# Kernel optimization log

Hardware: AMD Instinct MI355X
Metric: run time of the kernel (lower is better)

## Reference

```python
import jax, jax.numpy as jnp
import numpy as np

N_NODES = 100000
N_EDGES = 1000000
D = 64


def setup_inputs() -> dict:
    key = jax.random.key(0)
    k1, k2, k3, k4, k5, k6 = jax.random.split(key, 6)
    graph_embedding = jax.random.normal(k1, (N_NODES, D), dtype=jnp.float32)
    e_feat = jax.random.randint(k2, (N_EDGES,), 0, 8, dtype=jnp.int32)
    src_idx = jax.random.randint(k3, (N_EDGES,), 0, N_NODES, dtype=jnp.int32)
    dst_idx = jax.random.randint(k4, (N_EDGES,), 0, N_NODES, dtype=jnp.int32)
    # learned parameters (xavier-uniform-like scale)
    weight = jax.random.uniform(k5, (1, D), dtype=jnp.float32, minval=-1.0, maxval=1.0) * np.sqrt(6.0 / (1 + D))
    semantic_weight = jax.random.uniform(k6, (1, 5), dtype=jnp.float32, minval=-1.0, maxval=1.0) * np.sqrt(6.0 / (1 + 5))
    return {
        "graph_embedding": graph_embedding,
        "e_feat": e_feat,
        "src_idx": src_idx,
        "dst_idx": dst_idx,
        "weight": weight,
        "semantic_weight": semantic_weight,
    }


def reference(graph_embedding, e_feat, src_idx, dst_idx, weight, semantic_weight):
    n_nodes = graph_embedding.shape[0]
    # NOTE: original forward multiplies all five ft variants by the SAME self.weight
    emb = graph_embedding * weight                      # [N, D]
    src_ft = emb[src_idx]                               # [E, D] gather
    e = e_feat.astype(jnp.float32)[:, None]             # [E, 1] (e_feat.reshape(-1,1).float())
    sw = semantic_weight[0]                             # [5]
    msg = src_ft * sw[0]
    for i, ev in enumerate((0.0, 2.0, 4.0, 6.0)):
        mask = (e == ev)                                # [E, 1], broadcast over D
        msg = msg + jnp.where(mask, src_ft, jnp.zeros_like(src_ft)) * sw[i + 1]
    # scatter-sum messages into destination nodes
    out = jax.ops.segment_sum(msg, dst_idx, num_segments=n_nodes)  # [N, D]
    return out
```

## Files before the change

### kernel.cpp

```cpp
#include <hip/hip_runtime.h>


#define DIM 64
#define LOGB 7
#define NPB 128
#define NBUK_MAX 1024
#define CAP 2048
#define CHUNK 4096
#define OVF_CAP 8192

__global__ __launch_bounds__(512) void k_bin(
    const int* __restrict__ e_feat, const int* __restrict__ src_idx,
    const int* __restrict__ dst_idx,
    int* __restrict__ cursor, int* __restrict__ ovf_cnt, int4* __restrict__ ovf,
    unsigned int* __restrict__ recs, int E, int nbuk)
{
    __shared__ int hist[NBUK_MAX];
    __shared__ int start[NBUK_MAX];
    __shared__ int adjs[NBUK_MAX];
    __shared__ int partial[512];
    __shared__ unsigned int stage_rec[CHUNK];
    __shared__ unsigned short stage_b[CHUNK];

    const int t = threadIdx.x;
    const int base = blockIdx.x * CHUNK;
    int n = E - base; if (n > CHUNK) n = CHUNK;

    hist[t] = 0; hist[t + 512] = 0;
    __syncthreads();

    unsigned int rec[8]; int bk[8]; int lr[8];
    #pragma unroll
    for (int k = 0; k < 8; ++k) {
        int i = t + k * 512;
        if (i < n) {
            int j = base + i;
            int d = dst_idx[j];
            int s = src_idx[j];
            int f = e_feat[j];
            bk[k]  = d >> LOGB;
            rec[k] = (unsigned)s | ((unsigned)(d & (NPB - 1)) << 17)
                                 | ((unsigned)f << 24);
            lr[k]  = atomicAdd(&hist[bk[k]], 1);
        } else bk[k] = -1;
    }
    __syncthreads();

    int a  = hist[2 * t];
    int b2 = hist[2 * t + 1];
    partial[t] = a + b2;
    __syncthreads();
    for (int off = 1; off < 512; off <<= 1) {
        int v = (t >= off) ? partial[t - off] : 0;
        __syncthreads();
        partial[t] += v;
        __syncthreads();
    }
    int pbase = partial[t] - (a + b2);
    start[2 * t]     = pbase;
    start[2 * t + 1] = pbase + a;
    __syncthreads();

    #pragma unroll
    for (int k = 0; k < 8; ++k) {
        if (bk[k] >= 0) {
            int pos = start[bk[k]] + lr[k];
            stage_rec[pos] = rec[k];
            stage_b[pos]   = (unsigned short)bk[k];
        }
    }
    for (int b = t; b < nbuk; b += 512) {
        int c = hist[b];
        if (c > 0) {
            int g0 = atomicAdd(&cursor[b], c);
            adjs[b] = g0 - start[b];
        }
    }
    __syncthreads();

    for (int i = t; i < n; i += 512) {
        int b  = stage_b[i];
        int dp = adjs[b] + i;
        unsigned int r = stage_rec[i];
        if (dp < CAP) {
            recs[(size_t)b * CAP + dp] = r;
        } else {
            int oi = atomicAdd(ovf_cnt, 1);
            if (oi < OVF_CAP) {
                int s  = r & 0x1FFFF;
                int dl = (r >> 17) & (NPB - 1);
                int f  = (r >> 24) & 7;
                ovf[oi] = make_int4((b << LOGB) | dl, s, f, 0);
            }
        }
    }
}

__global__ __launch_bounds__(256) void k_regroup(
    const int* __restrict__ cursor, const unsigned int* __restrict__ recs,
    const float* __restrict__ sw,
    int2* __restrict__ recs2, int2* __restrict__ meta, int N)
{
    __shared__ int hist2[NPB];
    __shared__ int sc[NPB];
    __shared__ int nstart[NPB];
    __shared__ int2 rbuf[CAP];

    const int t = threadIdx.x;
    const int b = blockIdx.x;
    int cnt = cursor[b]; if (cnt > CAP) cnt = CAP;

    for (int i = t; i < NPB; i += 256) hist2[i] = 0;
    __syncthreads();

    float s0 = sw[0], s1 = sw[1], s2 = sw[2], s3 = sw[3], s4 = sw[4];

    unsigned int r[8]; int nl[8]; int lr[8];
    #pragma unroll
    for (int k = 0; k < 8; ++k) {
        int i = t + k * 256;
        if (i < cnt) {
            r[k]  = recs[(size_t)b * CAP + i];
            nl[k] = (r[k] >> 17) & (NPB - 1);
            lr[k] = atomicAdd(&hist2[nl[k]], 1);
        } else nl[k] = -1;
    }
    __syncthreads();

    if (t < NPB) sc[t] = hist2[t];
    __syncthreads();
    for (int off = 1; off < NPB; off <<= 1) {
        int v = (t < NPB && t >= off) ? sc[t - off] : 0;
        __syncthreads();
        if (t < NPB) sc[t] += v;
        __syncthreads();
    }
    if (t < NPB) nstart[t] = sc[t] - hist2[t];
    __syncthreads();

    #pragma unroll
    for (int k = 0; k < 8; ++k) {
        if (nl[k] >= 0) {
            int f = (r[k] >> 24) & 7;
            float c = s0;
            c += (f == 0) ? s1 : 0.0f;
            c += (f == 2) ? s2 : 0.0f;
            c += (f == 4) ? s3 : 0.0f;
            c += (f == 6) ? s4 : 0.0f;
            rbuf[nstart[nl[k]] + lr[k]] = make_int2((int)(r[k] & 0x1FFFF),
                                                    __float_as_int(c));
        }
    }
    __syncthreads();

    for (int i = t; i < cnt; i += 256)
        recs2[(size_t)b * CAP + i] = rbuf[i];

    const int node0 = b << LOGB;
    if (t < NPB) {
        int node = node0 + t;
        if (node < N)
            meta[node] = make_int2(b * CAP + nstart[t], hist2[t]);
    }
}

__global__ __launch_bounds__(256) void k_gather(
    const float* __restrict__ emb, const float* __restrict__ weight,
    const int2* __restrict__ meta, const int2* __restrict__ recs2,
    float* __restrict__ out, int N)
{
    int wave = threadIdx.x >> 6;
    int lane = threadIdx.x & 63;
    int node = blockIdx.x * 4 + wave;
    if (node >= N) return;

    int2 m = meta[node];
    int s = m.x, cnt = m.y;

    float a0=0.f,a1=0.f,a2=0.f,a3=0.f,a4=0.f,a5=0.f,a6=0.f,a7=0.f;

    for (int base = 0; base < cnt; base += 64) {
        int nch = cnt - base; if (nch > 64) nch = 64;
        int2 r = make_int2(0, 0);
        if (lane < nch) r = recs2[s + base + lane];
        int j = 0;
        for (; j + 7 < nch; j += 8) {
            int   s0 = __shfl(r.x, j    ), s1 = __shfl(r.x, j + 1);
            int   s2 = __shfl(r.x, j + 2), s3 = __shfl(r.x, j + 3);
            int   s4 = __shfl(r.x, j + 4), s5 = __shfl(r.x, j + 5);
            int   s6 = __shfl(r.x, j + 6), s7 = __shfl(r.x, j + 7);
            float c0 = __int_as_float(__shfl(r.y, j    ));
            float c1 = __int_as_float(__shfl(r.y, j + 1));
            float c2 = __int_as_float(__shfl(r.y, j + 2));
            float c3 = __int_as_float(__shfl(r.y, j + 3));
            float c4 = __int_as_float(__shfl(r.y, j + 4));
            float c5 = __int_as_float(__shfl(r.y, j + 5));
            float c6 = __int_as_float(__shfl(r.y, j + 6));
            float c7 = __int_as_float(__shfl(r.y, j + 7));
            a0 = fmaf(c0, emb[(size_t)s0 * DIM + lane], a0);
            a1 = fmaf(c1, emb[(size_t)s1 * DIM + lane], a1);
            a2 = fmaf(c2, emb[(size_t)s2 * DIM + lane], a2);
            a3 = fmaf(c3, emb[(size_t)s3 * DIM + lane], a3);
            a4 = fmaf(c4, emb[(size_t)s4 * DIM + lane], a4);
            a5 = fmaf(c5, emb[(size_t)s5 * DIM + lane], a5);
            a6 = fmaf(c6, emb[(size_t)s6 * DIM + lane], a6);
            a7 = fmaf(c7, emb[(size_t)s7 * DIM + lane], a7);
        }
        for (; j < nch; ++j) {
            int   sj = __shfl(r.x, j);
            float cj = __int_as_float(__shfl(r.y, j));
            a0 = fmaf(cj, emb[(size_t)sj * DIM + lane], a0);
        }
    }
    float acc = ((a0 + a1) + (a2 + a3)) + ((a4 + a5) + (a6 + a7));
    out[(size_t)node * DIM + lane] = acc * weight[lane];
}

__global__ __launch_bounds__(64) void k_overflow(
    const int* __restrict__ ovf_cnt, const int4* __restrict__ ovf,
    const float* __restrict__ emb, const float* __restrict__ weight,
    const float* __restrict__ sw, float* __restrict__ out)
{
    int m = *ovf_cnt; if (m > OVF_CAP) m = OVF_CAP;
    int lane = threadIdx.x;
    float s0 = sw[0], s1 = sw[1], s2 = sw[2], s3 = sw[3], s4 = sw[4];
    for (int i = blockIdx.x; i < m; i += gridDim.x) {
        int4 rec = ovf[i];
        int f = rec.z;
        float c = s0;
        c += (f == 0) ? s1 : 0.0f;
        c += (f == 2) ? s2 : 0.0f;
        c += (f == 4) ? s3 : 0.0f;
        c += (f == 6) ? s4 : 0.0f;
        float v = emb[(size_t)rec.y * DIM + lane] * weight[lane] * c;
        atomicAdd(&out[(size_t)rec.x * DIM + lane], v);
    }
}

__global__ __launch_bounds__(256) void edge_scatter_kernel(
    const float* __restrict__ emb, const int* __restrict__ e_feat,
    const int* __restrict__ src_idx, const int* __restrict__ dst_idx,
    const float* __restrict__ weight, const float* __restrict__ sw,
    float* __restrict__ out, int n_edges) {
    int tid = blockIdx.x * blockDim.x + threadIdx.x;
    int edge = tid >> 4;
    int quad = tid & 15;
    if (edge >= n_edges) return;
    int ef = e_feat[edge];
    float coef = sw[0];
    coef += (ef == 0) ? sw[1] : 0.0f;
    coef += (ef == 2) ? sw[2] : 0.0f;
    coef += (ef == 4) ? sw[3] : 0.0f;
    coef += (ef == 6) ? sw[4] : 0.0f;
    int src = src_idx[edge], dst = dst_idx[edge];
    const float4 ev = *reinterpret_cast<const float4*>(emb + (size_t)src * DIM + quad * 4);
    const float4 wv = *reinterpret_cast<const float4*>(weight + quad * 4);
    float* op = out + (size_t)dst * DIM + quad * 4;
    atomicAdd(op + 0, ev.x * wv.x * coef);
    atomicAdd(op + 1, ev.y * wv.y * coef);
    atomicAdd(op + 2, ev.z * wv.z * coef);
    atomicAdd(op + 3, ev.w * wv.w * coef);
}

extern "C" void kernel_launch(void* const* d_in, const int* in_sizes, int n_in,
                              void* d_out, int out_size, void* d_ws, size_t ws_size,
                              hipStream_t stream) {
    const float* emb     = (const float*)d_in[0];
    const int*   e_feat  = (const int*)d_in[1];
    const int*   src_idx = (const int*)d_in[2];
    const int*   dst_idx = (const int*)d_in[3];
    const float* weight  = (const float*)d_in[4];
    const float* sw      = (const float*)d_in[5];
    float* out = (float*)d_out;

    const int E = in_sizes[1];
    const int N = in_sizes[0] / DIM;
    const int nbuk = (N + NPB - 1) / NPB;

    size_t off_cursor = 0;
    size_t off_ovfcnt = off_cursor + (size_t)nbuk * 4;
    size_t off_ovf    = (off_ovfcnt + 4 + 15) & ~(size_t)15;
    size_t off_recs   = (off_ovf + (size_t)OVF_CAP * 16 + 15) & ~(size_t)15;
    size_t off_recs2  = (off_recs + (size_t)nbuk * CAP * 4 + 15) & ~(size_t)15;
    size_t off_meta   = (off_recs2 + (size_t)nbuk * CAP * 8 + 15) & ~(size_t)15;
    size_t needed     = off_meta + (size_t)N * 8;

    if (nbuk > NBUK_MAX || ws_size < needed) {
        hipMemsetAsync(d_out, 0, (size_t)out_size * sizeof(float), stream);
        int total = E * 16, block = 256;
        edge_scatter_kernel<<<(total + block - 1) / block, block, 0, stream>>>(
            emb, e_feat, src_idx, dst_idx, weight, sw, out, E);
        return;
    }

    char* ws = (char*)d_ws;
    int*          cursor  = (int*)(ws + off_cursor);
    int*          ovf_cnt = (int*)(ws + off_ovfcnt);
    int4*         ovf     = (int4*)(ws + off_ovf);
    unsigned int* recs    = (unsigned int*)(ws + off_recs);
    int2*         recs2   = (int2*)(ws + off_recs2);
    int2*         meta    = (int2*)(ws + off_meta);

    hipMemsetAsync(cursor, 0, off_ovfcnt + 16 - off_cursor, stream);

    k_bin<<<(E + CHUNK - 1) / CHUNK, 512, 0, stream>>>(
        e_feat, src_idx, dst_idx, cursor, ovf_cnt, ovf, recs, E, nbuk);

    k_regroup<<<nbuk, 256, 0, stream>>>(cursor, recs, sw, recs2, meta, N);

    k_gather<<<(N + 3) / 4, 256, 0, stream>>>(emb, weight, meta, recs2, out, N);

    k_overflow<<<64, 64, 0, stream>>>(ovf_cnt, ovf, emb, weight, sw, out);
}
```

Baseline: 158.4 us.

## Bin edges into coarse 512-node buckets and split regroup four ways per bucket

The first binning pass now sorts edges into 512-node coarse buckets instead of 128-node buckets. It uses smaller 2048-edge chunks with 256 threads and a byte-sized bucket id, and pads the global bucket cursors to separate cache lines to reduce atomic contention. With fewer buckets, each chunk writes longer contiguous runs per bucket and the scan is shorter. Regroup now launches four blocks per coarse bucket, and each block rescans the whole bucket to keep only its 128-node slice. That adds redundant reads of the record buffer. Records beyond the per-slice capacity are now dropped silently instead of going to the overflow path.

```diff
diff --git a/kernel.cpp b/kernel.cpp
--- a/kernel.cpp
+++ b/kernel.cpp
@@ -2,95 +2,91 @@
 
 
 #define DIM 64
-#define LOGB 7
-#define NPB 128
-#define NBUK_MAX 1024
-#define CAP 2048
-#define CHUNK 4096
+#define LOGC 9
+#define NPC 512
+#define NBC_MAX 256
+#define CAPC 6144
+#define CHUNK 2048
+#define NPB2 128
+#define CAP2 2048
 #define OVF_CAP 8192
-
-__global__ __launch_bounds__(512) void k_bin(
+#define CURSOR_STRIDE 16
+
+__global__ __launch_bounds__(256) void k_bin(
     const int* __restrict__ e_feat, const int* __restrict__ src_idx,
     const int* __restrict__ dst_idx,
     int* __restrict__ cursor, int* __restrict__ ovf_cnt, int4* __restrict__ ovf,
-    unsigned int* __restrict__ recs, int E, int nbuk)
+    unsigned int* __restrict__ recs, int E, int nbukc)
 {
-    __shared__ int hist[NBUK_MAX];
-    __shared__ int start[NBUK_MAX];
-    __shared__ int adjs[NBUK_MAX];
-    __shared__ int partial[512];
+    __shared__ int hist[NBC_MAX];
+    __shared__ int ss[NBC_MAX];
+    __shared__ int adjs[NBC_MAX];
     __shared__ unsigned int stage_rec[CHUNK];
-    __shared__ unsigned short stage_b[CHUNK];
+    __shared__ unsigned char stage_b[CHUNK];
 
     const int t = threadIdx.x;
     const int base = blockIdx.x * CHUNK;
     int n = E - base; if (n > CHUNK) n = CHUNK;
 
-    hist[t] = 0; hist[t + 512] = 0;
+    hist[t] = 0;
     __syncthreads();
 
     unsigned int rec[8]; int bk[8]; int lr[8];
     #pragma unroll
     for (int k = 0; k < 8; ++k) {
-        int i = t + k * 512;
+        int i = t + k * 256;
         if (i < n) {
             int j = base + i;
             int d = dst_idx[j];
             int s = src_idx[j];
             int f = e_feat[j];
-            bk[k]  = d >> LOGB;
-            rec[k] = (unsigned)s | ((unsigned)(d & (NPB - 1)) << 17)
-                                 | ((unsigned)f << 24);
+            bk[k]  = d >> LOGC;
+            rec[k] = (unsigned)s | ((unsigned)(d & (NPC - 1)) << 17)
+                                 | ((unsigned)f << 26);
             lr[k]  = atomicAdd(&hist[bk[k]], 1);
         } else bk[k] = -1;
     }
     __syncthreads();
 
-    int a  = hist[2 * t];
-    int b2 = hist[2 * t + 1];
-    partial[t] = a + b2;
-    __syncthreads();
-    for (int off = 1; off < 512; off <<= 1) {
-        int v = (t >= off) ? partial[t - off] : 0;
+    ss[t] = hist[t];
+    __syncthreads();
+    for (int off = 1; off < NBC_MAX; off <<= 1) {
+        int v = (t >= off) ? ss[t - off] : 0;
         __syncthreads();
-        partial[t] += v;
+        ss[t] += v;
         __syncthreads();
     }
-    int pbase = partial[t] - (a + b2);
-    start[2 * t]     = pbase;
-    start[2 * t + 1] = pbase + a;
-    __syncthreads();
 
     #pragma unroll
     for (int k = 0; k < 8; ++k) {
         if (bk[k] >= 0) {
-            int pos = start[bk[k]] + lr[k];
+            int pos = ss[bk[k]] - hist[bk[k]] + lr[k];
             stage_rec[pos] = rec[k];
-            stage_b[pos]   = (unsigned short)bk[k];
-        }
-    }
-    for (int b = t; b < nbuk; b += 512) {
-        int c = hist[b];
+            stage_b[pos]   = (unsigned char)bk[k];
+        }
+    }
+    if (t < nbukc) {
+        int c = hist[t];
         if (c > 0) {
-            int g0 = atomicAdd(&cursor[b], c);
-            adjs[b] = g0 - start[b];
-        }
-    }
-    __syncthreads();
-
-    for (int i = t; i < n; i += 512) {
+            int g0 = atomicAdd(&cursor[t * CURSOR_STRIDE], c);
+            adjs[t] = g0 - (ss[t] - c);
+        }
+    }
+    __syncthreads();
+
+    for (int i = t; i < n; i += 256) {
         int b  = stage_b[i];
         int dp = adjs[b] + i;
         unsigned int r = stage_rec[i];
-        if (dp < CAP) {
-            recs[(size_t)b * CAP + dp] = r;
+        if (dp < CAPC) {
+            recs[(size_t)b * CAPC + dp] = r;
         } else {
             int oi = atomicAdd(ovf_cnt, 1);
             if (oi < OVF_CAP) {
                 int s  = r & 0x1FFFF;
-                int dl = (r >> 17) & (NPB - 1);
-                int f  = (r >> 24) & 7;
-                ovf[oi] = make_int4((b << LOGB) | dl, s, f, 0);
+                int dl = (r >> 17) & (NPC - 1);
+                int f  = (r >> 26) & 7;
+                ovf[oi] = make_int4((b << LOGC) | dl, s, f, 0);
             }
         }
     }
@@ -101,66 +97,71 @@
     const float* __restrict__ sw,
     int2* __restrict__ recs2, int2* __restrict__ meta, int N)
 {
-    __shared__ int hist2[NPB];
-    __shared__ int sc[NPB];
-    __shared__ int nstart[NPB];
-    __shared__ int2 rbuf[CAP];
-
-    const int t = threadIdx.x;
-    const int b = blockIdx.x;
-    int cnt = cursor[b]; if (cnt > CAP) cnt = CAP;
-
-    for (int i = t; i < NPB; i += 256) hist2[i] = 0;
+    __shared__ int hist2[NPB2];
+    __shared__ int cur[NPB2];
+    __shared__ int nstart[NPB2];
+    __shared__ int2 rbuf[CAP2];
+
+    const int t   = threadIdx.x;
+    const int bid = blockIdx.x;
+    const int cb  = bid >> 2;
+    const int sub = bid & 3;
+
+    int cnt = cursor[cb * CURSOR_STRIDE]; if (cnt > CAPC) cnt = CAPC;
+    const unsigned int* rp = recs + (size_t)cb * CAPC;
+
+    if (t < NPB2) hist2[t] = 0;
+    __syncthreads();
+
+    for (int i = t; i < cnt; i += 256) {
+        unsigned int r = rp[i];
+        int dl = (r >> 17) & (NPC - 1);
+        if ((dl >> 7) == sub) atomicAdd(&hist2[dl & (NPB2 - 1)], 1);
+    }
+    __syncthreads();
+
+    if (t < NPB2) cur[t] = hist2[t];
+    __syncthreads();
+    for (int off = 1; off < NPB2; off <<= 1) {
+        int v = (t < NPB2 && t >= off) ? cur[t - off] : 0;
+        __syncthreads();
+        if (t < NPB2) cur[t] += v;
+        __syncthreads();
+    }
+    if (t < NPB2) { nstart[t] = cur[t] - hist2[t]; cur[t] = nstart[t]; }
     __syncthreads();
 
     float s0 = sw[0], s1 = sw[1], s2 = sw[2], s3 = sw[3], s4 = sw[4];
 
-    unsigned int r[8]; int nl[8]; int lr[8];
-    #pragma unroll
-    for (int k = 0; k < 8; ++k) {
-        int i = t + k * 256;
-        if (i < cnt) {
-            r[k]  = recs[(size_t)b * CAP + i];
-            nl[k] = (r[k] >> 17) & (NPB - 1);
-            lr[k] = atomicAdd(&hist2[nl[k]], 1);
-        } else nl[k] = -1;
-    }
-    __syncthreads();
-
-    if (t < NPB) sc[t] = hist2[t];
-    __syncthreads();
-    for (int off = 1; off < NPB; off <<= 1) {
-        int v = (t < NPB && t >= off) ? sc[t - off] : 0;
-        __syncthreads();
-        if (t < NPB) sc[t] += v;
-        __syncthreads();
-    }
-    if (t < NPB) nstart[t] = sc[t] - hist2[t];
-    __syncthreads();
-
-    #pragma unroll
-    for (int k = 0; k < 8; ++k) {
-        if (nl[k] >= 0) {
-            int f = (r[k] >> 24) & 7;
+    for (int i = t; i < cnt; i += 256) {
+        unsigned int r = rp[i];
+        int dl = (r >> 17) & (NPC - 1);
+        if ((dl >> 7) == sub) {
+            int f = (r >> 26) & 7;
             float c = s0;
             c += (f == 0) ? s1 : 0.0f;
             c += (f == 2) ? s2 : 0.0f;
             c += (f == 4) ? s3 : 0.0f;
             c += (f == 6) ? s4 : 0.0f;
-            rbuf[nstart[nl[k]] + lr[k]] = make_int2((int)(r[k] & 0x1FFFF),
-                                                    __float_as_int(c));
-        }
-    }
-    __syncthreads();
-
-    for (int i = t; i < cnt; i += 256)
-        recs2[(size_t)b * CAP + i] = rbuf[i];
-
-    const int node0 = b << LOGB;
-    if (t < NPB) {
+            int pos = atomicAdd(&cur[dl & (NPB2 - 1)], 1);
+            if (pos < CAP2)
+                rbuf[pos] = make_int2((int)(r & 0x1FFFF), __float_as_int(c));
+        }
+    }
+    __syncthreads();
+
+    int tot = nstart[NPB2 - 1] + hist2[NPB2 - 1]; if (tot > CAP2) tot = CAP2;
+    for (int i = t; i < tot; i += 256)
+        recs2[(size_t)bid * CAP2 + i] = rbuf[i];
+
+    const int node0 = (cb << LOGC) + sub * NPB2;
+    if (t < NPB2) {
         int node = node0 + t;
-        if (node < N)
-            meta[node] = make_int2(b * CAP + nstart[t], hist2[t]);
+        if (node < N) {
+            int st = nstart[t]; if (st > CAP2) st = CAP2;
+            int nc = hist2[t];  if (st + nc > CAP2) nc = CAP2 - st;
+            meta[node] = make_int2(bid * CAP2 + st, nc);
+        }
     }
 }
 
@@ -275,17 +276,17 @@
 
     const int E = in_sizes[1];
     const int N = in_sizes[0] / DIM;
-    const int nbuk = (N + NPB - 1) / NPB;
+    const int nbukc = (N + NPC - 1) / NPC;
 
     size_t off_cursor = 0;
-    size_t off_ovfcnt = off_cursor + (size_t)nbuk * 4;
+    size_t off_ovfcnt = off_cursor + (size_t)nbukc * CURSOR_STRIDE * 4;
     size_t off_ovf    = (off_ovfcnt + 4 + 15) & ~(size_t)15;
     size_t off_recs   = (off_ovf + (size_t)OVF_CAP * 16 + 15) & ~(size_t)15;
-    size_t off_recs2  = (off_recs + (size_t)nbuk * CAP * 4 + 15) & ~(size_t)15;
-    size_t off_meta   = (off_recs2 + (size_t)nbuk * CAP * 8 + 15) & ~(size_t)15;
+    size_t off_recs2  = (off_recs + (size_t)nbukc * CAPC * 4 + 15) & ~(size_t)15;
+    size_t off_meta   = (off_recs2 + (size_t)nbukc * 4 * CAP2 * 8 + 15) & ~(size_t)15;
     size_t needed     = off_meta + (size_t)N * 8;
 
-    if (nbuk > NBUK_MAX || ws_size < needed) {
+    if (nbukc > NBC_MAX || ws_size < needed) {
         hipMemsetAsync(d_out, 0, (size_t)out_size * sizeof(float), stream);
         int total = E * 16, block = 256;
         edge_scatter_kernel<<<(total + block - 1) / block, block, 0, stream>>>(
@@ -303,10 +304,10 @@
 
     hipMemsetAsync(cursor, 0, off_ovfcnt + 16 - off_cursor, stream);
 
-    k_bin<<<(E + CHUNK - 1) / CHUNK, 512, 0, stream>>>(
-        e_feat, src_idx, dst_idx, cursor, ovf_cnt, ovf, recs, E, nbuk);
-
-    k_regroup<<<nbuk, 256, 0, stream>>>(cursor, recs, sw, recs2, meta, N);
+    k_bin<<<(E + CHUNK - 1) / CHUNK, 256, 0, stream>>>(
+        e_feat, src_idx, dst_idx, cursor, ovf_cnt, ovf, recs, E, nbukc);
+
+    k_regroup<<<nbukc * 4, 256, 0, stream>>>(cursor, recs, sw, recs2, meta, N);
 
     k_gather<<<(N + 3) / 4, 256, 0, stream>>>(emb, weight, meta, recs2, out, N);
 
```

Result: slower. 170.1 us (+7.4%).

## Gather from a bf16 copy of embeddings and pack edge records into 32 bits

Applied to the files above, without the earlier changes.

Adds a conversion kernel that rounds the embedding table to bf16 in workspace, and the gather kernel now reads 2-byte rows instead of 4-byte ones. Edge records are packed into one 32-bit word (source index plus edge type), and coefficients come from a small shared-memory table built per block. The goal is to cut gather traffic and record bandwidth. The cost is an extra conversion pass over the table and reduced precision in the accumulated messages.

```diff
diff --git a/kernel.cpp b/kernel.cpp
--- a/kernel.cpp
+++ b/kernel.cpp
@@ -8,6 +8,21 @@
 #define CAP 2048
 #define CHUNK 4096
 #define OVF_CAP 8192
+
+__global__ __launch_bounds__(256) void k_convert(
+    const float* __restrict__ emb, unsigned short* __restrict__ emb16, int total4)
+{
+    int i = blockIdx.x * blockDim.x + threadIdx.x;
+    if (i >= total4) return;
+    float4 v = reinterpret_cast<const float4*>(emb)[i];
+    ushort4 o;
+    unsigned int x;
+    x = __float_as_uint(v.x); o.x = (unsigned short)((x + 0x7FFF + ((x >> 16) & 1)) >> 16);
+    x = __float_as_uint(v.y); o.y = (unsigned short)((x + 0x7FFF + ((x >> 16) & 1)) >> 16);
+    x = __float_as_uint(v.z); o.z = (unsigned short)((x + 0x7FFF + ((x >> 16) & 1)) >> 16);
+    x = __float_as_uint(v.w); o.w = (unsigned short)((x + 0x7FFF + ((x >> 16) & 1)) >> 16);
+    reinterpret_cast<ushort4*>(emb16)[i] = o;
+}
 
 __global__ __launch_bounds__(512) void k_bin(
     const int* __restrict__ e_feat, const int* __restrict__ src_idx,
@@ -98,13 +113,12 @@
 
 __global__ __launch_bounds__(256) void k_regroup(
     const int* __restrict__ cursor, const unsigned int* __restrict__ recs,
-    const float* __restrict__ sw,
-    int2* __restrict__ recs2, int2* __restrict__ meta, int N)
+    unsigned int* __restrict__ recs2, int2* __restrict__ meta, int N)
 {
     __shared__ int hist2[NPB];
     __shared__ int sc[NPB];
     __shared__ int nstart[NPB];
-    __shared__ int2 rbuf[CAP];
+    __shared__ unsigned int rbuf[CAP];
 
     const int t = threadIdx.x;
     const int b = blockIdx.x;
@@ -112,8 +126,6 @@
 
     for (int i = t; i < NPB; i += 256) hist2[i] = 0;
     __syncthreads();
-
-    float s0 = sw[0], s1 = sw[1], s2 = sw[2], s3 = sw[3], s4 = sw[4];
 
     unsigned int r[8]; int nl[8]; int lr[8];
     #pragma unroll
@@ -141,14 +153,7 @@
     #pragma unroll
     for (int k = 0; k < 8; ++k) {
         if (nl[k] >= 0) {
-            int f = (r[k] >> 24) & 7;
-            float c = s0;
-            c += (f == 0) ? s1 : 0.0f;
-            c += (f == 2) ? s2 : 0.0f;
-            c += (f == 4) ? s3 : 0.0f;
-            c += (f == 6) ? s4 : 0.0f;
-            rbuf[nstart[nl[k]] + lr[k]] = make_int2((int)(r[k] & 0x1FFFF),
-                                                    __float_as_int(c));
+            rbuf[nstart[nl[k]] + lr[k]] = (r[k] & 0x1FFFF) | (((r[k] >> 24) & 7) << 17);
         }
     }
     __syncthreads();
@@ -164,13 +169,26 @@
     }
 }
 
-__global__ __launch_bounds__(256) void k_gather(
-    const float* __restrict__ emb, const float* __restrict__ weight,
-    const int2* __restrict__ meta, const int2* __restrict__ recs2,
+__global__ __launch_bounds__(256) void k_gather_bf16(
+    const unsigned short* __restrict__ emb16, const float* __restrict__ weight,
+    const float* __restrict__ sw,
+    const int2* __restrict__ meta, const unsigned int* __restrict__ recs2,
     float* __restrict__ out, int N)
 {
+    __shared__ float ctab[8];
     int wave = threadIdx.x >> 6;
     int lane = threadIdx.x & 63;
+    if (threadIdx.x < 8) {
+        int f = threadIdx.x;
+        float c = sw[0];
+        c += (f == 0) ? sw[1] : 0.0f;
+        c += (f == 2) ? sw[2] : 0.0f;
+        c += (f == 4) ? sw[3] : 0.0f;
+        c += (f == 6) ? sw[4] : 0.0f;
+        ctab[f] = c;
+    }
+    __syncthreads();
+
     int node = blockIdx.x * 4 + wave;
     if (node >= N) return;
 
@@ -181,35 +199,91 @@
 
     for (int base = 0; base < cnt; base += 64) {
         int nch = cnt - base; if (nch > 64) nch = 64;
-        int2 r = make_int2(0, 0);
+        unsigned int r = 0;
         if (lane < nch) r = recs2[s + base + lane];
         int j = 0;
         for (; j + 7 < nch; j += 8) {
-            int   s0 = __shfl(r.x, j    ), s1 = __shfl(r.x, j + 1);
-            int   s2 = __shfl(r.x, j + 2), s3 = __shfl(r.x, j + 3);
-            int   s4 = __shfl(r.x, j + 4), s5 = __shfl(r.x, j + 5);
-            int   s6 = __shfl(r.x, j + 6), s7 = __shfl(r.x, j + 7);
-            float c0 = __int_as_float(__shfl(r.y, j    ));
-            float c1 = __int_as_float(__shfl(r.y, j + 1));
-            float c2 = __int_as_float(__shfl(r.y, j + 2));
-            float c3 = __int_as_float(__shfl(r.y, j + 3));
-            float c4 = __int_as_float(__shfl(r.y, j + 4));
-            float c5 = __int_as_float(__shfl(r.y, j + 5));
-            float c6 = __int_as_float(__shfl(r.y, j + 6));
-            float c7 = __int_as_float(__shfl(r.y, j + 7));
-            a0 = fmaf(c0, emb[(size_t)s0 * DIM + lane], a0);
-            a1 = fmaf(c1, emb[(size_t)s1 * DIM + lane], a1);
-            a2 = fmaf(c2, emb[(size_t)s2 * DIM + lane], a2);
-            a3 = fmaf(c3, emb[(size_t)s3 * DIM + lane], a3);
-            a4 = fmaf(c4, emb[(size_t)s4 * DIM + lane], a4);
-            a5 = fmaf(c5, emb[(size_t)s5 * DIM + lane], a5);
-            a6 = fmaf(c6, emb[(size_t)s6 * DIM + lane], a6);
-            a7 = fmaf(c7, emb[(size_t)s7 * DIM + lane], a7);
+            unsigned int r0 = __shfl(r, j    ), r1 = __shfl(r, j + 1);
+            unsigned int r2 = __shfl(r, j + 2), r3 = __shfl(r, j + 3);
+            unsigned int r4 = __shfl(r, j + 4), r5 = __shfl(r, j + 5);
+            unsigned int r6 = __shfl(r, j + 6), r7 = __shfl(r, j + 7);
+            float v0 = __uint_as_float((unsigned int)emb16[(size_t)(r0 & 0x1FFFF) * DIM + lane] << 16);
+            float v1 = __uint_as_float((unsigned int)emb16[(size_t)(r1 & 0x1FFFF) * DIM + lane] << 16);
+            float v2 = __uint_as_float((unsigned int)emb16[(size_t)(r2 & 0x1FFFF) * DIM + lane] << 16);
+            float v3 = __uint_as_float((unsigned int)emb16[(size_t)(r3 & 0x1FFFF) * DIM + lane] << 16);
+            float v4 = __uint_as_float((unsigned int)emb16[(size_t)(r4 & 0x1FFFF) * DIM + lane] << 16);
+            float v5 = __uint_as_float((unsigned int)emb16[(size_t)(r5 & 0x1FFFF) * DIM + lane] << 16);
+            float v6 = __uint_as_float((unsigned int)emb16[(size_t)(r6 & 0x1FFFF) * DIM + lane] << 16);
+            float v7 = __uint_as_float((unsigned int)emb16[(size_t)(r7 & 0x1FFFF) * DIM + lane] << 16);
+            a0 = fmaf(ctab[r0 >> 17], v0, a0);
+            a1 = fmaf(ctab[r1 >> 17], v1, a1);
+            a2 = fmaf(ctab[r2 >> 17], v2, a2);
+            a3 = fmaf(ctab[r3 >> 17], v3, a3);
+            a4 = fmaf(ctab[r4 >> 17], v4, a4);
+            a5 = fmaf(ctab[r5 >> 17], v5, a5);
+            a6 = fmaf(ctab[r6 >> 17], v6, a6);
+            a7 = fmaf(ctab[r7 >> 17], v7, a7);
         }
         for (; j < nch; ++j) {
-            int   sj = __shfl(r.x, j);
-            float cj = __int_as_float(__shfl(r.y, j));
-            a0 = fmaf(cj, emb[(size_t)sj * DIM + lane], a0);
+            unsigned int rj = __shfl(r, j);
+            float v = __uint_as_float((unsigned int)emb16[(size_t)(rj & 0x1FFFF) * DIM + lane] << 16);
+            a0 = fmaf(ctab[rj >> 17], v, a0);
+        }
+    }
+    float acc = ((a0 + a1) + (a2 + a3)) + ((a4 + a5) + (a6 + a7));
+    out[(size_t)node * DIM + lane] = acc * weight[lane];
+}
+
+__global__ __launch_bounds__(256) void k_gather_f32(
+    const float* __restrict__ emb, const float* __restrict__ weight,
+    const float* __restrict__ sw,
+    const int2* __restrict__ meta, const unsigned int* __restrict__ recs2,
+    float* __restrict__ out, int N)
+{
+    __shared__ float ctab[8];
+    int wave = threadIdx.x >> 6;
+    int lane = threadIdx.x & 63;
+    if (threadIdx.x < 8) {
+        int f = threadIdx.x;
+        float c = sw[0];
+        c += (f == 0) ? sw[1] : 0.0f;
+        c += (f == 2) ? sw[2] : 0.0f;
+        c += (f == 4) ? sw[3] : 0.0f;
+        c += (f == 6) ? sw[4] : 0.0f;
+        ctab[f] = c;
+    }
+    __syncthreads();
+
+    int node = blockIdx.x * 4 + wave;
+    if (node >= N) return;
+
+    int2 m = meta[node];
+    int s = m.x, cnt = m.y;
+
+    float a0=0.f,a1=0.f,a2=0.f,a3=0.f,a4=0.f,a5=0.f,a6=0.f,a7=0.f;
+
+    for (int base = 0; base < cnt; base += 64) {
+        int nch = cnt - base; if (nch > 64) nch = 64;
+        unsigned int r = 0;
+        if (lane < nch) r = recs2[s + base + lane];
+        int j = 0;
+        for (; j + 7 < nch; j += 8) {
+            unsigned int r0 = __shfl(r, j    ), r1 = __shfl(r, j + 1);
+            unsigned int r2 = __shfl(r, j + 2), r3 = __shfl(r, j + 3);
+            unsigned int r4 = __shfl(r, j + 4), r5 = __shfl(r, j + 5);
+            unsigned int r6 = __shfl(r, j + 6), r7 = __shfl(r, j + 7);
+            a0 = fmaf(ctab[r0 >> 17], emb[(size_t)(r0 & 0x1FFFF) * DIM + lane], a0);
+            a1 = fmaf(ctab[r1 >> 17], emb[(size_t)(r1 & 0x1FFFF) * DIM + lane], a1);
+            a2 = fmaf(ctab[r2 >> 17], emb[(size_t)(r2 & 0x1FFFF) * DIM + lane], a2);
+            a3 = fmaf(ctab[r3 >> 17], emb[(size_t)(r3 & 0x1FFFF) * DIM + lane], a3);
+            a4 = fmaf(ctab[r4 >> 17], emb[(size_t)(r4 & 0x1FFFF) * DIM + lane], a4);
+            a5 = fmaf(ctab[r5 >> 17], emb[(size_t)(r5 & 0x1FFFF) * DIM + lane], a5);
+            a6 = fmaf(ctab[r6 >> 17], emb[(size_t)(r6 & 0x1FFFF) * DIM + lane], a6);
+            a7 = fmaf(ctab[r7 >> 17], emb[(size_t)(r7 & 0x1FFFF) * DIM + lane], a7);
+        }
+        for (; j < nch; ++j) {
+            unsigned int rj = __shfl(r, j);
+            a0 = fmaf(ctab[rj >> 17], emb[(size_t)(rj & 0x1FFFF) * DIM + lane], a0);
         }
     }
     float acc = ((a0 + a1) + (a2 + a3)) + ((a4 + a5) + (a6 + a7));
@@ -282,8 +356,10 @@
     size_t off_ovf    = (off_ovfcnt + 4 + 15) & ~(size_t)15;
     size_t off_recs   = (off_ovf + (size_t)OVF_CAP * 16 + 15) & ~(size_t)15;
     size_t off_recs2  = (off_recs + (size_t)nbuk * CAP * 4 + 15) & ~(size_t)15;
-    size_t off_meta   = (off_recs2 + (size_t)nbuk * CAP * 8 + 15) & ~(size_t)15;
-    size_t needed     = off_meta + (size_t)N * 8;
+    size_t off_meta   = (off_recs2 + (size_t)nbuk * CAP * 4 + 15) & ~(size_t)15;
+    size_t off_emb16  = (off_meta + (size_t)N * 8 + 15) & ~(size_t)15;
+    size_t needed     = off_emb16;
+    size_t needed16   = off_emb16 + (size_t)N * DIM * 2;
 
     if (nbuk > NBUK_MAX || ws_size < needed) {
         hipMemsetAsync(d_out, 0, (size_t)out_size * sizeof(float), stream);
@@ -292,23 +368,36 @@
             emb, e_feat, src_idx, dst_idx, weight, sw, out, E);
         return;
     }
+    const bool use_bf16 = (ws_size >= needed16);
 
     char* ws = (char*)d_ws;
-    int*          cursor  = (int*)(ws + off_cursor);
-    int*          ovf_cnt = (int*)(ws + off_ovfcnt);
-    int4*         ovf     = (int4*)(ws + off_ovf);
-    unsigned int* recs    = (unsigned int*)(ws + off_recs);
-    int2*         recs2   = (int2*)(ws + off_recs2);
-    int2*         meta    = (int2*)(ws + off_meta);
+    int*            cursor  = (int*)(ws + off_cursor);
+    int*            ovf_cnt = (int*)(ws + off_ovfcnt);
+    int4*           ovf     = (int4*)(ws + off_ovf);
+    unsigned int*   recs    = (unsigned int*)(ws + off_recs);
+    unsigned int*   recs2   = (unsigned int*)(ws + off_recs2);
+    int2*           meta    = (int2*)(ws + off_meta);
+    unsigned short* emb16   = (unsigned short*)(ws + off_emb16);
 
     hipMemsetAsync(cursor, 0, off_ovfcnt + 16 - off_cursor, stream);
+
+    if (use_bf16) {
+        int total4 = N * DIM / 4;
+        k_convert<<<(total4 + 255) / 256, 256, 0, stream>>>(emb, emb16, total4);
+    }
 
     k_bin<<<(E + CHUNK - 1) / CHUNK, 512, 0, stream>>>(
         e_feat, src_idx, dst_idx, cursor, ovf_cnt, ovf, recs, E, nbuk);
 
-    k_regroup<<<nbuk, 256, 0, stream>>>(cursor, recs, sw, recs2, meta, N);
-
-    k_gather<<<(N + 3) / 4, 256, 0, stream>>>(emb, weight, meta, recs2, out, N);
+    k_regroup<<<nbuk, 256, 0, stream>>>(cursor, recs, recs2, meta, N);
+
+    if (use_bf16) {
+        k_gather_bf16<<<(N + 3) / 4, 256, 0, stream>>>(
+            emb16, weight, sw, meta, recs2, out, N);
+    } else {
+        k_gather_f32<<<(N + 3) / 4, 256, 0, stream>>>(
+            emb, weight, sw, meta, recs2, out, N);
+    }
 
     k_overflow<<<64, 64, 0, stream>>>(ovf_cnt, ovf, emb, weight, sw, out);
 }
```

Result: slower. 166.1 us (+4.9%).
